# Kernel tuning notes

Hardware: AMD Instinct MI355X
Metric: run time of the kernel (lower is better)

The kernel has to match this reference:

```python
import jax, jax.numpy as jnp
import numpy as np

NUM_HEADS = 16


def setup_inputs() -> dict:
    key = jax.random.key(0)
    ks = jax.random.split(key, 7)
    T, B, E = 2048, 2, 1024
    s = 0.02
    return {
        "query": jax.random.normal(ks[0], (T, B, E), jnp.float32),
        "key": jax.random.normal(ks[1], (T, B, E), jnp.float32),
        "value": jax.random.normal(ks[2], (T, B, E), jnp.float32),
        "in_proj_weight": jax.random.normal(ks[3], (3 * E, E), jnp.float32) * s,
        "in_proj_bias": jax.random.normal(ks[4], (3 * E,), jnp.float32) * s,
        "out_proj_weight": jax.random.normal(ks[5], (E, E), jnp.float32) * s,
        "out_proj_bias": jax.random.normal(ks[6], (E,), jnp.float32) * s,
    }


def reference(query, key, value, in_proj_weight, in_proj_bias,
              out_proj_weight, out_proj_bias):
    T, B, E = query.shape
    H = NUM_HEADS
    Dh = E // H
    Wq, Wk, Wv = jnp.split(in_proj_weight, 3, axis=0)   # each (E, E)
    bq, bk, bv = jnp.split(in_proj_bias, 3, axis=0)
    # packed in-projection (F._in_projection_packed)
    q = query @ Wq.T + bq   # (T, B, E)
    k = key @ Wk.T + bk
    v = value @ Wv.T + bv
    # (T, B, E) -> (B, H, T, Dh)
    def to_heads(x):
        return x.reshape(T, B, H, Dh).transpose(1, 2, 0, 3)
    q, k, v = to_heads(q), to_heads(k), to_heads(v)
    scale = 1.0 / jnp.sqrt(jnp.asarray(Dh, q.dtype))
    scores = jnp.einsum('bhtd,bhsd->bhts', q, k) * scale  # (B, H, T, T)
    attn = jax.nn.softmax(scores, axis=-1)
    ctx = jnp.einsum('bhts,bhsd->bhtd', attn, v)          # (B, H, T, Dh)
    # (B, H, T, Dh) -> (T, B, E)
    ctx = ctx.transpose(2, 0, 1, 3).reshape(T, B, E)
    out = ctx @ out_proj_weight.T + out_proj_bias          # (T, B, E)
    return out
```

## Files before the change

kernel.cpp:

```cpp
#include <hip/hip_runtime.h>
#include <stdint.h>


typedef __bf16 bf16;
typedef __bf16 bf16x8 __attribute__((ext_vector_type(8)));
typedef float f32x4 __attribute__((ext_vector_type(4)));
typedef unsigned int u32x4 __attribute__((ext_vector_type(4)));

#define MFMA16(a, b, c) __builtin_amdgcn_mfma_f32_16x16x32_bf16((a), (b), (c), 0, 0, 0)

static __device__ __forceinline__ void gload_lds16(const void* g, void* lds) {
  __builtin_amdgcn_global_load_lds(
      (__attribute__((address_space(1))) void*)(g),
      (__attribute__((address_space(3))) void*)(lds), 16u, 0, 0u);
}

static __device__ __forceinline__ unsigned pack2_bf16(float a, float b) {
  unsigned short ua = __builtin_bit_cast(unsigned short, (bf16)a);
  unsigned short ub = __builtin_bit_cast(unsigned short, (bf16)b);
  return (unsigned)ua | ((unsigned)ub << 16);
}

__global__ __launch_bounds__(256) void cvt5_kernel(
    const float* __restrict__ s0, const float* __restrict__ s1,
    const float* __restrict__ s2, const float* __restrict__ s3,
    const float* __restrict__ s4,
    bf16* __restrict__ d0, bf16* __restrict__ d1, bf16* __restrict__ d2,
    bf16* __restrict__ d3, bf16* __restrict__ d4) {
  const int y = blockIdx.y;
  const float* s; bf16* d; int n8;
  switch (y) {
    case 0: s = s0; d = d0; n8 = 524288; break;
    case 1: s = s1; d = d1; n8 = 524288; break;
    case 2: s = s2; d = d2; n8 = 524288; break;
    case 3: s = s3; d = d3; n8 = 393216; break;
    default: s = s4; d = d4; n8 = 131072; break;
  }
  const int i = blockIdx.x * 256 + threadIdx.x;
  if (i >= n8) return;
  const float4* sp = reinterpret_cast<const float4*>(s) + (size_t)i * 2;
  float4 a = sp[0], b = sp[1];
  bf16x8 o;
  o[0] = (bf16)a.x; o[1] = (bf16)a.y; o[2] = (bf16)a.z; o[3] = (bf16)a.w;
  o[4] = (bf16)b.x; o[5] = (bf16)b.y; o[6] = (bf16)b.z; o[7] = (bf16)b.w;
  *reinterpret_cast<bf16x8*>(d + (size_t)i * 8) = o;
}

__global__ __launch_bounds__(256) void vtrans_kernel(const bf16* __restrict__ v,
                                                     bf16* __restrict__ vt) {
  __shared__ bf16 tile[64][65];
  const int bh = blockIdx.y;
  const int t0 = blockIdx.x * 64;
  const int r = threadIdx.x >> 2;
  const int c0 = (threadIdx.x & 3) * 16;
  const bf16* src = v + ((size_t)bh * 2048 + t0 + r) * 64 + c0;
  bf16x8 a = *reinterpret_cast<const bf16x8*>(src);
  bf16x8 b = *reinterpret_cast<const bf16x8*>(src + 8);
#pragma unroll
  for (int j = 0; j < 8; ++j) tile[c0 + j][r] = a[j];
#pragma unroll
  for (int j = 0; j < 8; ++j) tile[c0 + 8 + j][r] = b[j];
  __syncthreads();
  bf16x8 o1, o2;
#pragma unroll
  for (int j = 0; j < 8; ++j) o1[j] = tile[r][c0 + j];
#pragma unroll
  for (int j = 0; j < 8; ++j) o2[j] = tile[r][c0 + 8 + j];
  bf16* dst = vt + ((size_t)bh * 64 + r) * 2048 + t0 + c0;
  *reinterpret_cast<bf16x8*>(dst) = o1;
  *reinterpret_cast<bf16x8*>(dst + 8) = o2;
}

static __device__ __forceinline__ void gemm_tile_compute(
    const bf16* Ab, const bf16* Bb, int wm, int wn, int g, int c15,
    f32x4 (&acc)[4][4]) {
  bf16x8 af[4], bfr[4];
#pragma unroll
  for (int mi = 0; mi < 4; ++mi)
    af[mi] = *reinterpret_cast<const bf16x8*>(Ab + (((wm * 4 + mi) * 4 + g) * 16 + c15) * 8);
#pragma unroll
  for (int ni = 0; ni < 4; ++ni)
    bfr[ni] = *reinterpret_cast<const bf16x8*>(Bb + (((wn * 4 + ni) * 4 + g) * 16 + c15) * 8);
#pragma unroll
  for (int mi = 0; mi < 4; ++mi)
#pragma unroll
    for (int ni = 0; ni < 4; ++ni)
      acc[mi][ni] = MFMA16(af[mi], bfr[ni], acc[mi][ni]);
}

static __device__ __forceinline__ void gemm_core_128x128(
    const bf16* __restrict__ A, const bf16* __restrict__ Bw, int K,
    bf16* Alds, bf16* Blds, f32x4 (&acc)[4][4]) {
  const int tid = threadIdx.x;
  const int wid = tid >> 6, lane = tid & 63;
  const int g = lane >> 4, c15 = lane & 15;
  const int wm = wid >> 1, wn = wid & 1;
#pragma unroll
  for (int mi = 0; mi < 4; ++mi)
#pragma unroll
    for (int ni = 0; ni < 4; ++ni) acc[mi][ni] = f32x4{0.f, 0.f, 0.f, 0.f};

  const int u0 = tid, u1 = 256 + tid;
  const int row0 = ((u0 >> 6) << 4) + (u0 & 15), col0 = ((u0 >> 4) & 3) * 8;
  const int row1 = ((u1 >> 6) << 4) + (u1 & 15), col1 = ((u1 >> 4) & 3) * 8;
  const bf16* ga0 = A + (size_t)row0 * K + col0;
  const bf16* ga1 = A + (size_t)row1 * K + col1;
  const bf16* gb0 = Bw + (size_t)row0 * K + col0;
  const bf16* gb1 = Bw + (size_t)row1 * K + col1;
  const int lofs0 = wid * 512, lofs1 = 2048 + wid * 512;

#define GSTAGE(kt, buf) do {                                   \
    gload_lds16(ga0 + (kt), Alds + (buf) * 4096 + lofs0);      \
    gload_lds16(ga1 + (kt), Alds + (buf) * 4096 + lofs1);      \
    gload_lds16(gb0 + (kt), Blds + (buf) * 4096 + lofs0);      \
    gload_lds16(gb1 + (kt), Blds + (buf) * 4096 + lofs1);      \
  } while (0)

  GSTAGE(0, 0);
  __syncthreads();
  int cur = 0;
  for (int kt = 32; kt < K; kt += 32) {
    GSTAGE(kt, cur ^ 1);
    gemm_tile_compute(Alds + cur * 4096, Blds + cur * 4096, wm, wn, g, c15, acc);
    __syncthreads();
    cur ^= 1;
  }
  gemm_tile_compute(Alds + cur * 4096, Blds + cur * 4096, wm, wn, g, c15, acc);
#undef GSTAGE
}

__global__ __launch_bounds__(256) void gemm_inproj(
    const bf16* __restrict__ xq, const bf16* __restrict__ xk, const bf16* __restrict__ xv,
    const bf16* __restrict__ w, const float* __restrict__ bias,
    bf16* __restrict__ qo, bf16* __restrict__ ko, bf16* __restrict__ vo) {
  __shared__ __align__(16) bf16 Alds[2 * 4096];
  __shared__ __align__(16) bf16 Blds[2 * 4096];
  const int m0 = blockIdx.x * 128, n0 = blockIdx.y * 128;
  const int tensor = n0 >> 10;
  const bf16* A = (tensor == 0 ? xq : tensor == 1 ? xk : xv) + (size_t)m0 * 1024;
  const bf16* Bw = w + (size_t)n0 * 1024;
  f32x4 acc[4][4];
  gemm_core_128x128(A, Bw, 1024, Alds, Blds, acc);

  const int lane = threadIdx.x & 63, wid = threadIdx.x >> 6;
  const int g = lane >> 4, c15 = lane & 15;
  const int wm = wid >> 1, wn = wid & 1;
  const float QS = 0.18033688011112042f;
  bf16* dst = tensor == 0 ? qo : tensor == 1 ? ko : vo;
  const float scale = tensor == 0 ? QS : 1.0f;
#pragma unroll
  for (int mi = 0; mi < 4; ++mi)
#pragma unroll
    for (int ni = 0; ni < 4; ++ni) {
      const int n = n0 + wn * 64 + ni * 16 + c15;
      const float bn = bias[n];
      const int h = (n >> 6) & 15, d = n & 63;
#pragma unroll
      for (int r = 0; r < 4; ++r) {
        const int m = m0 + wm * 64 + mi * 16 + 4 * g + r;
        const int t = m >> 1, b = m & 1;
        const int bh = b * 16 + h;
        dst[((size_t)bh * 2048 + t) * 64 + d] = (bf16)((acc[mi][ni][r] + bn) * scale);
      }
    }
}

__global__ __launch_bounds__(256) void gemm_outproj(
    const bf16* __restrict__ ctx, const bf16* __restrict__ w,
    const float* __restrict__ bias, float* __restrict__ out) {
  __shared__ __align__(16) bf16 Alds[2 * 2048];
  __shared__ __align__(16) bf16 Blds[2 * 4096];
  const int m0 = blockIdx.x * 64, n0 = blockIdx.y * 128;
  const int tid = threadIdx.x;
  const int wid = tid >> 6, lane = tid & 63;
  const int g = lane >> 4, c15 = lane & 15;
  const int wm = wid >> 1, wn = wid & 1;
  f32x4 acc[2][4];
#pragma unroll
  for (int mi = 0; mi < 2; ++mi)
#pragma unroll
    for (int ni = 0; ni < 4; ++ni) acc[mi][ni] = f32x4{0.f, 0.f, 0.f, 0.f};

  const int u0 = tid, u1 = 256 + tid;
  const int row0 = ((u0 >> 6) << 4) + (u0 & 15), col0 = ((u0 >> 4) & 3) * 8;
  const int row1 = ((u1 >> 6) << 4) + (u1 & 15), col1 = ((u1 >> 4) & 3) * 8;
  const bf16* ga0 = ctx + (size_t)(m0 + row0) * 1024 + col0;
  const bf16* gb0 = w + (size_t)(n0 + row0) * 1024 + col0;
  const bf16* gb1 = w + (size_t)(n0 + row1) * 1024 + col1;

#define OSTAGE(kt, buf) do {                                        \
    gload_lds16(ga0 + (kt), Alds + (buf) * 2048 + wid * 512);       \
    gload_lds16(gb0 + (kt), Blds + (buf) * 4096 + wid * 512);       \
    gload_lds16(gb1 + (kt), Blds + (buf) * 4096 + 2048 + wid * 512);\
  } while (0)

  OSTAGE(0, 0);
  __syncthreads();
  int cur = 0;
  for (int kt = 32; kt < 1024; kt += 32) {
    OSTAGE(kt, cur ^ 1);
    {
      const bf16* Ab = Alds + cur * 2048;
      const bf16* Bb = Blds + cur * 4096;
      bf16x8 af[2], bfr[4];
#pragma unroll
      for (int mi = 0; mi < 2; ++mi)
        af[mi] = *reinterpret_cast<const bf16x8*>(Ab + (((wm * 2 + mi) * 4 + g) * 16 + c15) * 8);
#pragma unroll
      for (int ni = 0; ni < 4; ++ni)
        bfr[ni] = *reinterpret_cast<const bf16x8*>(Bb + (((wn * 4 + ni) * 4 + g) * 16 + c15) * 8);
#pragma unroll
      for (int mi = 0; mi < 2; ++mi)
#pragma unroll
        for (int ni = 0; ni < 4; ++ni)
          acc[mi][ni] = MFMA16(af[mi], bfr[ni], acc[mi][ni]);
    }
    __syncthreads();
    cur ^= 1;
  }
  {
    const bf16* Ab = Alds + cur * 2048;
    const bf16* Bb = Blds + cur * 4096;
    bf16x8 af[2], bfr[4];
#pragma unroll
    for (int mi = 0; mi < 2; ++mi)
      af[mi] = *reinterpret_cast<const bf16x8*>(Ab + (((wm * 2 + mi) * 4 + g) * 16 + c15) * 8);
#pragma unroll
    for (int ni = 0; ni < 4; ++ni)
      bfr[ni] = *reinterpret_cast<const bf16x8*>(Bb + (((wn * 4 + ni) * 4 + g) * 16 + c15) * 8);
#pragma unroll
    for (int mi = 0; mi < 2; ++mi)
#pragma unroll
      for (int ni = 0; ni < 4; ++ni)
        acc[mi][ni] = MFMA16(af[mi], bfr[ni], acc[mi][ni]);
  }
#undef OSTAGE

#pragma unroll
  for (int mi = 0; mi < 2; ++mi)
#pragma unroll
    for (int ni = 0; ni < 4; ++ni) {
      const int n = n0 + wn * 64 + ni * 16 + c15;
      const float bn = bias[n];
#pragma unroll
      for (int r = 0; r < 4; ++r) {
        const int m = m0 + wm * 32 + mi * 16 + 4 * g + r;
        out[(size_t)m * 1024 + n] = acc[mi][ni][r] + bn;
      }
    }
}

static __device__ __forceinline__ void softmax_dist(
    const f32x4 (&sc)[4], int g, int c15, int ghi,
    bf16x8& pvf0, bf16x8& pvf1) {
  float p[4][4];
#pragma unroll
  for (int c = 0; c < 4; ++c)
#pragma unroll
    for (int r = 0; r < 4; ++r) p[c][r] = __builtin_amdgcn_exp2f(sc[c][r]);

  unsigned pk[4][2];
#pragma unroll
  for (int c = 0; c < 4; ++c) {
    pk[c][0] = pack2_bf16(p[c][0], p[c][1]);
    pk[c][1] = pack2_bf16(p[c][2], p[c][3]);
  }
  u32x4 pvu[2];
#pragma unroll
  for (int kkv = 0; kkv < 2; ++kkv) {
    unsigned wrec[2][2];
#pragma unroll
    for (int u = 0; u < 2; ++u)
#pragma unroll
      for (int v = 0; v < 2; ++v) {
        const unsigned val = ((g & 1) ^ u) ? pk[kkv * 2 + 1][v] : pk[kkv * 2][v];
        wrec[u][v] = __shfl(val, ((g & 1) * 2 + ((g >> 1) ^ u)) * 16 + c15);
      }
    pvu[kkv][0] = ghi ? wrec[1][0] : wrec[0][0];
    pvu[kkv][1] = ghi ? wrec[1][1] : wrec[0][1];
    pvu[kkv][2] = ghi ? wrec[0][0] : wrec[1][0];
    pvu[kkv][3] = ghi ? wrec[0][1] : wrec[1][1];
  }
  pvf0 = __builtin_bit_cast(bf16x8, pvu[0]);
  pvf1 = __builtin_bit_cast(bf16x8, pvu[1]);
}

__global__ __launch_bounds__(256, 2) void attn_kernel(
    const bf16* __restrict__ q, const bf16* __restrict__ k,
    const bf16* __restrict__ vt, bf16* __restrict__ ctx) {
  __shared__ __align__(16) bf16 Klds[2 * 4096];
  __shared__ __align__(16) bf16 Vlds[2 * 4096];
  const int tid = threadIdx.x;
  const int wid = tid >> 6, lane = tid & 63;
  const int g = lane >> 4, c15 = lane & 15;
  const int ghi = (g >> 1) & 1;
  const int bh = blockIdx.y;
  const int q0 = blockIdx.x * 128;
  const size_t headoff = (size_t)bh * 2048 * 64;

  const bf16* qrow0 = q + headoff + (size_t)(q0 + wid * 32 + c15) * 64;
  const bf16* qrow1 = qrow0 + 16 * 64;
  const bf16x8 qf0a = *reinterpret_cast<const bf16x8*>(qrow0 + 8 * g);
  const bf16x8 qf0b = *reinterpret_cast<const bf16x8*>(qrow0 + 32 + 8 * g);
  const bf16x8 qf1a = *reinterpret_cast<const bf16x8*>(qrow1 + 8 * g);
  const bf16x8 qf1b = *reinterpret_cast<const bf16x8*>(qrow1 + 32 + 8 * g);

  f32x4 acc0[4], acc1[4], accl0, accl1;
#pragma unroll
  for (int i = 0; i < 4; ++i) {
    acc0[i] = f32x4{0.f, 0.f, 0.f, 0.f};
    acc1[i] = f32x4{0.f, 0.f, 0.f, 0.f};
  }
  accl0 = f32x4{0.f, 0.f, 0.f, 0.f};
  accl1 = f32x4{0.f, 0.f, 0.f, 0.f};
  bf16x8 ones;
#pragma unroll
  for (int j = 0; j < 8; ++j) ones[j] = (bf16)1.0f;

  const int u0 = tid, u1 = 256 + tid;
  const int row0 = ((u0 >> 7) << 4) + (u0 & 15), col0 = ((u0 >> 6) & 1) * 32 + ((u0 >> 4) & 3) * 8;
  const int row1 = ((u1 >> 7) << 4) + (u1 & 15), col1 = ((u1 >> 6) & 1) * 32 + ((u1 >> 4) & 3) * 8;
  const bf16* kbase = k + headoff;
  const bf16* vbase = vt + headoff;
  const int lofs0 = wid * 512, lofs1 = 2048 + wid * 512;

#define ASTAGE(kt, buf) do {                                                        \
    const int kv0_ = (kt) * 64;                                                     \
    gload_lds16(kbase + (size_t)(kv0_ + row0) * 64 + col0, Klds + (buf) * 4096 + lofs0); \
    gload_lds16(kbase + (size_t)(kv0_ + row1) * 64 + col1, Klds + (buf) * 4096 + lofs1); \
    gload_lds16(vbase + (size_t)row0 * 2048 + kv0_ + col0, Vlds + (buf) * 4096 + lofs0); \
    gload_lds16(vbase + (size_t)row1 * 2048 + kv0_ + col1, Vlds + (buf) * 4096 + lofs1); \
  } while (0)

  ASTAGE(0, 0);
  __syncthreads();
  int cur = 0;

  for (int kt = 0; kt < 32; ++kt) {
    if (kt < 31) ASTAGE(kt + 1, cur ^ 1);
    const bf16* Kb = Klds + cur * 4096;
    const bf16* Vb = Vlds + cur * 4096;

    f32x4 sc0[4], sc1[4];
    __builtin_amdgcn_s_setprio(1);
#pragma unroll
    for (int c = 0; c < 4; ++c) {
      const bf16x8 kf0 = *reinterpret_cast<const bf16x8*>(Kb + (((c * 2 + 0) * 4 + g) * 16 + c15) * 8);
      const bf16x8 kf1 = *reinterpret_cast<const bf16x8*>(Kb + (((c * 2 + 1) * 4 + g) * 16 + c15) * 8);
      const f32x4 z = f32x4{0.f, 0.f, 0.f, 0.f};
      sc0[c] = MFMA16(kf1, qf0b, MFMA16(kf0, qf0a, z));
      sc1[c] = MFMA16(kf1, qf1b, MFMA16(kf0, qf1a, z));
    }
    __builtin_amdgcn_s_setprio(0);

    bf16x8 pa0, pb0, pa1, pb1;
    softmax_dist(sc0, g, c15, ghi, pa0, pb0);
    softmax_dist(sc1, g, c15, ghi, pa1, pb1);

    __builtin_amdgcn_s_setprio(1);
#pragma unroll
    for (int dc = 0; dc < 4; ++dc) {
      const bf16x8 vf0 = *reinterpret_cast<const bf16x8*>(Vb + (((dc * 2 + 0) * 4 + g) * 16 + c15) * 8);
      const bf16x8 vf1 = *reinterpret_cast<const bf16x8*>(Vb + (((dc * 2 + 1) * 4 + g) * 16 + c15) * 8);
      acc0[dc] = MFMA16(vf1, pb0, MFMA16(vf0, pa0, acc0[dc]));
      acc1[dc] = MFMA16(vf1, pb1, MFMA16(vf0, pa1, acc1[dc]));
    }
    accl0 = MFMA16(ones, pb0, MFMA16(ones, pa0, accl0));
    accl1 = MFMA16(ones, pb1, MFMA16(ones, pa1, accl1));
    __builtin_amdgcn_s_setprio(0);

    __syncthreads();
    cur ^= 1;
  }
#undef ASTAGE

  const int b = bh >> 4, h = bh & 15;
  const int t0 = q0 + wid * 32 + c15;
  {
    const float rinv = 1.0f / accl0[0];
    bf16* cbase = ctx + (size_t)(t0 * 2 + b) * 1024 + h * 64;
#pragma unroll
    for (int dc = 0; dc < 4; ++dc)
#pragma unroll
      for (int r = 0; r < 4; ++r)
        cbase[dc * 16 + 4 * g + r] = (bf16)(acc0[dc][r] * rinv);
  }
  {
    const float rinv = 1.0f / accl1[0];
    bf16* cbase = ctx + (size_t)((t0 + 16) * 2 + b) * 1024 + h * 64;
#pragma unroll
    for (int dc = 0; dc < 4; ++dc)
#pragma unroll
      for (int r = 0; r < 4; ++r)
        cbase[dc * 16 + 4 * g + r] = (bf16)(acc1[dc][r] * rinv);
  }
}

extern "C" void kernel_launch(void* const* d_in, const int* in_sizes, int n_in,
                              void* d_out, int out_size, void* d_ws, size_t ws_size,
                              hipStream_t stream) {
  const float* query = (const float*)d_in[0];
  const float* key   = (const float*)d_in[1];
  const float* value = (const float*)d_in[2];
  const float* in_w  = (const float*)d_in[3];
  const float* in_b  = (const float*)d_in[4];
  const float* out_w = (const float*)d_in[5];
  const float* out_b = (const float*)d_in[6];

  bf16* ws = (bf16*)d_ws;
  const size_t M4 = 4194304;
  bf16* xq  = ws;
  bf16* xk  = xq + M4;
  bf16* xv  = xk + M4;
  bf16* wi  = xv + M4;
  bf16* wo  = wi + 3145728;
  bf16* qh  = wo + 1048576;
  bf16* kh  = qh + M4;
  bf16* vh  = kh + M4;
  bf16* ctx = vh + M4;
  bf16* vth = xq;

  cvt5_kernel<<<dim3(2048, 5), 256, 0, stream>>>(query, key, value, in_w, out_w,
                                                 xq, xk, xv, wi, wo);
  gemm_inproj<<<dim3(32, 24), 256, 0, stream>>>(xq, xk, xv, wi, in_b, qh, kh, vh);
  vtrans_kernel<<<dim3(32, 32), 256, 0, stream>>>(vh, vth);
  attn_kernel<<<dim3(16, 32), 256, 0, stream>>>(qh, kh, vth, ctx);
  gemm_outproj<<<dim3(64, 8), 256, 0, stream>>>(ctx, wo, out_b, (float*)d_out);
}
```

Measured before the change: 251.7 us.

## Split KV range across two wave groups per attention block and reduce via LDS

The attention block grows from 256 to 512 threads. Each half of the waves processes half of the 2048 keys for the same 128 queries, with its own double-buffered K/V staging in LDS. Afterwards the second half writes its partial output accumulators and row sums to LDS, and the first half adds them and writes the normalized context. This doubles resident waves and halves each wave's serial KV loop, to hide latency better. The cost is twice the LDS footprint, an extra barrier and an LDS reduction at the end.

```diff
diff --git a/kernel.cpp b/kernel.cpp
--- a/kernel.cpp
+++ b/kernel.cpp
@@ -285,20 +285,21 @@
   pvf1 = __builtin_bit_cast(bf16x8, pvu[1]);
 }
 
-__global__ __launch_bounds__(256, 2) void attn_kernel(
+__global__ __launch_bounds__(512, 4) void attn_kernel(
     const bf16* __restrict__ q, const bf16* __restrict__ k,
     const bf16* __restrict__ vt, bf16* __restrict__ ctx) {
-  __shared__ __align__(16) bf16 Klds[2 * 4096];
-  __shared__ __align__(16) bf16 Vlds[2 * 4096];
+  __shared__ __align__(16) bf16 Klds[4 * 4096];
+  __shared__ __align__(16) bf16 Vlds[4 * 4096];
   const int tid = threadIdx.x;
   const int wid = tid >> 6, lane = tid & 63;
+  const int wq = wid & 3, half = wid >> 2;
   const int g = lane >> 4, c15 = lane & 15;
   const int ghi = (g >> 1) & 1;
   const int bh = blockIdx.y;
   const int q0 = blockIdx.x * 128;
   const size_t headoff = (size_t)bh * 2048 * 64;
 
-  const bf16* qrow0 = q + headoff + (size_t)(q0 + wid * 32 + c15) * 64;
+  const bf16* qrow0 = q + headoff + (size_t)(q0 + wq * 32 + c15) * 64;
   const bf16* qrow1 = qrow0 + 16 * 64;
   const bf16x8 qf0a = *reinterpret_cast<const bf16x8*>(qrow0 + 8 * g);
   const bf16x8 qf0b = *reinterpret_cast<const bf16x8*>(qrow0 + 32 + 8 * g);
@@ -317,29 +318,32 @@
 #pragma unroll
   for (int j = 0; j < 8; ++j) ones[j] = (bf16)1.0f;
 
-  const int u0 = tid, u1 = 256 + tid;
+  const int htid = tid & 255;
+  const int u0 = htid, u1 = 256 + htid;
   const int row0 = ((u0 >> 7) << 4) + (u0 & 15), col0 = ((u0 >> 6) & 1) * 32 + ((u0 >> 4) & 3) * 8;
   const int row1 = ((u1 >> 7) << 4) + (u1 & 15), col1 = ((u1 >> 6) & 1) * 32 + ((u1 >> 4) & 3) * 8;
   const bf16* kbase = k + headoff;
   const bf16* vbase = vt + headoff;
-  const int lofs0 = wid * 512, lofs1 = 2048 + wid * 512;
+  const int lofs0 = wq * 512, lofs1 = 2048 + wq * 512;
 
 #define ASTAGE(kt, buf) do {                                                        \
-    const int kv0_ = (kt) * 64;                                                     \
-    gload_lds16(kbase + (size_t)(kv0_ + row0) * 64 + col0, Klds + (buf) * 4096 + lofs0); \
-    gload_lds16(kbase + (size_t)(kv0_ + row1) * 64 + col1, Klds + (buf) * 4096 + lofs1); \
-    gload_lds16(vbase + (size_t)row0 * 2048 + kv0_ + col0, Vlds + (buf) * 4096 + lofs0); \
-    gload_lds16(vbase + (size_t)row1 * 2048 + kv0_ + col1, Vlds + (buf) * 4096 + lofs1); \
+    const int kv0_ = (half * 16 + (kt)) * 64;                                       \
+    bf16* Kd = Klds + (half * 2 + (buf)) * 4096;                                    \
+    bf16* Vd = Vlds + (half * 2 + (buf)) * 4096;                                    \
+    gload_lds16(kbase + (size_t)(kv0_ + row0) * 64 + col0, Kd + lofs0);             \
+    gload_lds16(kbase + (size_t)(kv0_ + row1) * 64 + col1, Kd + lofs1);             \
+    gload_lds16(vbase + (size_t)row0 * 2048 + kv0_ + col0, Vd + lofs0);             \
+    gload_lds16(vbase + (size_t)row1 * 2048 + kv0_ + col1, Vd + lofs1);             \
   } while (0)
 
   ASTAGE(0, 0);
   __syncthreads();
   int cur = 0;
 
-  for (int kt = 0; kt < 32; ++kt) {
-    if (kt < 31) ASTAGE(kt + 1, cur ^ 1);
-    const bf16* Kb = Klds + cur * 4096;
-    const bf16* Vb = Vlds + cur * 4096;
+  for (int kt = 0; kt < 16; ++kt) {
+    if (kt < 15) ASTAGE(kt + 1, cur ^ 1);
+    const bf16* Kb = Klds + (half * 2 + cur) * 4096;
+    const bf16* Vb = Vlds + (half * 2 + cur) * 4096;
 
     f32x4 sc0[4], sc1[4];
     __builtin_amdgcn_s_setprio(1);
@@ -374,25 +378,46 @@
   }
 #undef ASTAGE
 
-  const int b = bh >> 4, h = bh & 15;
-  const int t0 = q0 + wid * 32 + c15;
-  {
-    const float rinv = 1.0f / accl0[0];
-    bf16* cbase = ctx + (size_t)(t0 * 2 + b) * 1024 + h * 64;
-#pragma unroll
-    for (int dc = 0; dc < 4; ++dc)
-#pragma unroll
-      for (int r = 0; r < 4; ++r)
-        cbase[dc * 16 + 4 * g + r] = (bf16)(acc0[dc][r] * rinv);
-  }
-  {
-    const float rinv = 1.0f / accl1[0];
-    bf16* cbase = ctx + (size_t)((t0 + 16) * 2 + b) * 1024 + h * 64;
-#pragma unroll
-    for (int dc = 0; dc < 4; ++dc)
-#pragma unroll
-      for (int r = 0; r < 4; ++r)
-        cbase[dc * 16 + 4 * g + r] = (bf16)(acc1[dc][r] * rinv);
+  float* ex  = reinterpret_cast<float*>(Klds);
+  float* exl = reinterpret_cast<float*>(Vlds);
+  if (half == 1) {
+#pragma unroll
+    for (int dc = 0; dc < 4; ++dc) {
+      *reinterpret_cast<f32x4*>(ex + ((wq * 8 + dc) * 64 + lane) * 4) = acc0[dc];
+      *reinterpret_cast<f32x4*>(ex + ((wq * 8 + 4 + dc) * 64 + lane) * 4) = acc1[dc];
+    }
+    exl[(wq * 2 + 0) * 64 + lane] = accl0[0];
+    exl[(wq * 2 + 1) * 64 + lane] = accl1[0];
+  }
+  __syncthreads();
+  if (half == 0) {
+#pragma unroll
+    for (int dc = 0; dc < 4; ++dc) {
+      acc0[dc] += *reinterpret_cast<const f32x4*>(ex + ((wq * 8 + dc) * 64 + lane) * 4);
+      acc1[dc] += *reinterpret_cast<const f32x4*>(ex + ((wq * 8 + 4 + dc) * 64 + lane) * 4);
+    }
+    const float l0 = accl0[0] + exl[(wq * 2 + 0) * 64 + lane];
+    const float l1 = accl1[0] + exl[(wq * 2 + 1) * 64 + lane];
+    const int b = bh >> 4, h = bh & 15;
+    const int t0q = q0 + wq * 32 + c15;
+    {
+      const float rinv = 1.0f / l0;
+      bf16* cbase = ctx + (size_t)(t0q * 2 + b) * 1024 + h * 64;
+#pragma unroll
+      for (int dc = 0; dc < 4; ++dc)
+#pragma unroll
+        for (int r = 0; r < 4; ++r)
+          cbase[dc * 16 + 4 * g + r] = (bf16)(acc0[dc][r] * rinv);
+    }
+    {
+      const float rinv = 1.0f / l1;
+      bf16* cbase = ctx + (size_t)((t0q + 16) * 2 + b) * 1024 + h * 64;
+#pragma unroll
+      for (int dc = 0; dc < 4; ++dc)
+#pragma unroll
+        for (int r = 0; r < 4; ++r)
+          cbase[dc * 16 + 4 * g + r] = (bf16)(acc1[dc][r] * rinv);
+    }
   }
 }
 
@@ -424,6 +449,6 @@
                                                  xq, xk, xv, wi, wo);
   gemm_inproj<<<dim3(32, 24), 256, 0, stream>>>(xq, xk, xv, wi, in_b, qh, kh, vh);
   vtrans_kernel<<<dim3(32, 32), 256, 0, stream>>>(vh, vth);
-  attn_kernel<<<dim3(16, 32), 256, 0, stream>>>(qh, kh, vth, ctx);
+  attn_kernel<<<dim3(16, 32), 512, 0, stream>>>(qh, kh, vth, ctx);
   gemm_outproj<<<dim3(64, 8), 256, 0, stream>>>(ctx, wo, out_b, (float*)d_out);
 }
```

New measurement: 245.8 us. 1.02x faster.
